# Optimization experiments

Measured on AMD Instinct MI355X. Metric: run time of the kernel, lower is better.

The kernel has to match this reference:

```python
import jax, jax.numpy as jnp
import numpy as np

NH = 8          # num_heads
NEG = -1e30     # mask_logits fill value


def setup_inputs() -> dict:
    key = jax.random.key(0)
    k1, k2, k3, k4 = jax.random.split(key, 4)
    B, D, T = 4, 1024, 2048
    x = jax.random.normal(k1, (B, D, T), dtype=jnp.float32)
    mask = jax.random.randint(k2, (B, T), 0, 2).astype(jnp.float32)
    # xavier-uniform-ish linear weights, torch layout [out, in]
    lim = float(np.sqrt(6.0 / (D + D)))
    Wq = jax.random.uniform(k3, (D, D), dtype=jnp.float32, minval=-lim, maxval=lim)
    Wo = jax.random.uniform(k4, (D, D), dtype=jnp.float32, minval=-lim, maxval=lim)
    return {"x": x, "mask": mask, "Wq": Wq, "Wo": Wo}


def reference(x, mask, Wq, Wo):
    # x: [B, D, T] channels-first; mask: [B, T] in {0,1} float
    B, D, T = x.shape
    dk = D // NH
    scale = 1.0 / jnp.sqrt(jnp.asarray(dk, x.dtype))
    xt = jnp.transpose(x, (0, 2, 1))                 # [B, T, D]
    # NOTE: original source uses Wqs for Q, K and V (source bug, reproduced)
    q = xt @ Wq.T                                    # [B, T, D]
    qh = q.reshape(B, T, NH, dk).transpose(0, 2, 1, 3)  # [B, H, T, dk]
    scores = scale * jnp.einsum('bhqd,bhkd->bhqk', qh, qh)  # [B, H, T, T]
    cmask = mask[:, None, None, :]                   # column mask [B,1,1,T]
    rmask = mask[:, None, :, None]                   # row mask    [B,1,T,1]
    logits = (scores * cmask + (1.0 - cmask) * NEG) * rmask
    attn = jax.nn.softmax(logits, axis=-1)
    ctx = jnp.einsum('bhqk,bhkd->bhqd', attn, qh)    # [B, H, T, dk]
    ctx = ctx.transpose(0, 2, 1, 3).reshape(B, T, D)
    out = ctx @ Wo.T                                 # [B, T, D]
    return jnp.transpose(out, (0, 2, 1))             # [B, D, T]
```

## Files before the change

kernel.cpp:

```cpp
#include <hip/hip_runtime.h>

#define TT 2048
#define DD 1024
#define NHH 8
#define DKK 128
#define SCALE2 0.1275174724f

typedef __attribute__((ext_vector_type(8)))  short short8;
typedef __attribute__((ext_vector_type(4)))  short short4v;
typedef __attribute__((ext_vector_type(4)))  float float4v;
typedef __attribute__((ext_vector_type(16))) float float16v;
typedef __attribute__((ext_vector_type(4)))  int   int4v;

__device__ __forceinline__ short f2bf(float f) {
  union { float f; unsigned u; } v; v.f = f;
  unsigned r = v.u + 0x7FFFu + ((v.u >> 16) & 1u);
  return (short)(r >> 16);
}
__device__ __forceinline__ unsigned cvtpk(float lo, float hi) {
  unsigned r;
  asm("v_cvt_pk_bf16_f32 %0, %1, %2" : "=v"(r) : "v"(lo), "v"(hi));
  return r;
}
__device__ __forceinline__ float xhalf_add(float x) {
  float y;
  asm("v_mov_b32 %0, %1" : "=v"(y) : "v"(x));
  asm("v_permlane32_swap_b32 %0, %1" : "+v"(x), "+v"(y));
  return x + y;
}
__device__ __forceinline__ int s4(int row) {
  return (row & 7) ^ (((row >> 3) & 3) << 2);
}
__device__ __forceinline__ void gl2lds(const void* g, void* l) {
  __builtin_amdgcn_global_load_lds(
      (const __attribute__((address_space(1))) void*)g,
      (__attribute__((address_space(3))) void*)l, 16, 0, 0);
}

__global__ __launch_bounds__(256) void k_xt(const float* __restrict__ x,
                                            short* __restrict__ xt) {
  __shared__ float tile[32][33];
  int b = blockIdx.z, d0 = blockIdx.y << 5, t0 = blockIdx.x << 5;
  int tx = threadIdx.x & 31, ty = threadIdx.x >> 5;
  const float* xp = x + ((size_t)b * DD + d0) * TT + t0;
#pragma unroll
  for (int yy = 0; yy < 32; yy += 8)
    tile[ty + yy][tx] = xp[(size_t)(ty + yy) * TT + tx];
  __syncthreads();
  short* op = xt + ((size_t)b * TT + t0) * DD + d0;
#pragma unroll
  for (int yy = 0; yy < 32; yy += 8)
    op[(size_t)(ty + yy) * DD + tx] = f2bf(tile[tx][ty + yy]);
}

__global__ void k_cast(const float* __restrict__ w, short* __restrict__ o, int n4) {
  int i = blockIdx.x * 256 + threadIdx.x;
  if (i < n4) {
    float4v v = ((const float4v*)w)[i];
    short4v s;
#pragma unroll
    for (int j = 0; j < 4; ++j) s[j] = f2bf(v[j]);
    ((short4v*)o)[i] = s;
  }
}

__global__ __launch_bounds__(256) void k_qt(const short* __restrict__ qb,
                                            short* __restrict__ qhT) {
  __shared__ short tile[64][65];
  int b = blockIdx.z, n0 = blockIdx.y << 6, t0 = blockIdx.x << 6;
  int tx = threadIdx.x & 63, ty = threadIdx.x >> 6;
  const short* ip = qb + ((size_t)(b * TT + t0)) * DD + n0;
#pragma unroll
  for (int yy = 0; yy < 64; yy += 4)
    tile[ty + yy][tx] = ip[(size_t)(ty + yy) * DD + tx];
  __syncthreads();
  short* op = qhT + ((size_t)(b * DD + n0)) * TT + t0;
#pragma unroll
  for (int yy = 0; yy < 64; yy += 4)
    op[(size_t)(ty + yy) * TT + tx] = tile[tx][ty + yy];
}

template <int EPI>
__global__ __launch_bounds__(256) void k_gemm(const short* __restrict__ A,
                                              const short* __restrict__ Bt,
                                              void* __restrict__ Cout) {
  __shared__ __align__(16) short As[128 * 64];
  __shared__ __align__(16) short Bs[128 * 64];
  const int K = 1024;
  int tm = blockIdx.x * 128, tn = blockIdx.y * 128;
  int tid = threadIdx.x, lane = tid & 63, w = tid >> 6;
  int wm = (w >> 1) * 64, wn = (w & 1) * 64;
  int ql = lane & 15, g = lane >> 4;

  int srow[4], scol[4];
#pragma unroll
  for (int c = 0; c < 4; ++c) {
    int cg = w * 4 + c;
    int r = cg * 8 + (lane >> 3);
    srow[c] = r;
    scol[c] = ((lane & 7) ^ (r & 7)) * 8;
  }

  float4v acc[4][4];
#pragma unroll
  for (int mt = 0; mt < 4; ++mt)
#pragma unroll
    for (int nt = 0; nt < 4; ++nt) acc[mt][nt] = (float4v){0.f, 0.f, 0.f, 0.f};

  for (int k0 = 0; k0 < K; k0 += 64) {
    __syncthreads();
#pragma unroll
    for (int c = 0; c < 4; ++c) {
      int cg = w * 4 + c;
      gl2lds(A + (size_t)(tm + srow[c]) * K + k0 + scol[c], As + cg * 512);
      gl2lds(Bt + (size_t)(tn + srow[c]) * K + k0 + scol[c], Bs + cg * 512);
    }
    __syncthreads();
#pragma unroll
    for (int k4 = 0; k4 < 2; ++k4) {
      short8 af[4], bfr[4];
#pragma unroll
      for (int mt = 0; mt < 4; ++mt) {
        int row = wm + mt * 16 + ql;
        af[mt] = *(const short8*)(As + row * 64 + (((k4 * 4 + g) ^ (ql & 7)) * 8));
      }
#pragma unroll
      for (int nt = 0; nt < 4; ++nt) {
        int row = wn + nt * 16 + ql;
        bfr[nt] = *(const short8*)(Bs + row * 64 + (((k4 * 4 + g) ^ (ql & 7)) * 8));
      }
#pragma unroll
      for (int mt = 0; mt < 4; ++mt)
#pragma unroll
        for (int nt = 0; nt < 4; ++nt)
          acc[mt][nt] = __builtin_amdgcn_mfma_f32_16x16x32_bf16(af[mt], bfr[nt],
                                                                acc[mt][nt], 0, 0, 0);
    }
  }

#pragma unroll
  for (int mt = 0; mt < 4; ++mt)
#pragma unroll
    for (int nt = 0; nt < 4; ++nt)
#pragma unroll
      for (int r = 0; r < 4; ++r) {
        int m = tm + wm + mt * 16 + g * 4 + r;
        int n = tn + wn + nt * 16 + ql;
        float v = acc[mt][nt][r];
        if (EPI == 0) {
          ((short*)Cout)[(size_t)m * 1024 + n] = f2bf(v);
        } else {
          int b = n >> 11, t = n & 2047;
          ((float*)Cout)[((size_t)b * 1024 + m) * 2048 + t] = v;
        }
      }
}

__global__ __launch_bounds__(256, 2) void k_attn(const short* __restrict__ q,
                                                 const short* __restrict__ qhT,
                                                 const float* __restrict__ mask,
                                                 short* __restrict__ ctx) {
  __shared__ __align__(16) short Ks[2][64 * 128];
  __shared__ __align__(16) short Vt[2][128 * 64];
  __shared__ __align__(16) short Kx[2][64 * 16];

  int qt = blockIdx.x, bh = blockIdx.y;
  int b = bh >> 3, h = bh & 7;
  int tid = threadIdx.x, lane = tid & 63, w = tid >> 6;
  int ql32 = lane & 31, hi = lane >> 5;
  int csw = s4(ql32);
  int vsw = ql32 & 7;
  short negbig = f2bf(-1e30f);

  int qrow = qt * 128 + w * 32 + ql32;
  const short* qp = q + ((size_t)(b * TT + qrow)) * DD + h * DKK;
  short8 qf[8];
#pragma unroll
  for (int kc8 = 0; kc8 < 8; ++kc8)
    qf[kc8] = *(const short8*)(qp + kc8 * 16 + hi * 8);
  float rm = mask[(size_t)b * TT + qrow];

  float qs = SCALE2 * rm;
#pragma unroll
  for (int kc8 = 0; kc8 < 8; ++kc8) {
    union { short8 s; unsigned u[4]; } a;
    a.s = qf[kc8];
#pragma unroll
    for (int j = 0; j < 4; ++j) {
      union { unsigned u; float f; } lo, hh;
      lo.u = a.u[j] << 16;
      hh.u = a.u[j] & 0xFFFF0000u;
      a.u[j] = cvtpk(lo.f * qs, hh.f * qs);
    }
    qf[kc8] = a.s;
  }
  short8 bext = (short8)0;
  if (hi == 0) bext[0] = (rm != 0.f) ? (short)0x3F80 : (short)0;

  int oc = tid & 15, r2 = tid >> 4;
  const short* kbase_g = q + ((size_t)b * TT) * DD + h * DKK + oc * 8;
  const short* vbase_g = qhT + ((size_t)(b * DD + h * DKK)) * TT;
  int vd[4], vko[4], vwoff[4];
#pragma unroll
  for (int p = 0; p < 4; ++p) {
    int idx = p * 256 + tid;
    vd[p] = idx >> 3;
    vko[p] = idx & 7;
    vwoff[p] = vd[p] * 64 + ((vko[p] ^ (vd[p] & 7)) * 8);
  }
  int kwoff[2][2];
#pragma unroll
  for (int ps = 0; ps < 2; ++ps) {
    int ra = 2 * r2 + 32 * ps, rb = ra + 1;
    kwoff[ps][0] = ra * 128 + ((oc ^ s4(ra)) * 8);
    kwoff[ps][1] = rb * 128 + ((oc ^ s4(rb)) * 8);
  }

  short8 va[2], vb[2], vv[4];
#pragma unroll
  for (int ps = 0; ps < 2; ++ps) {
    const short* kp = kbase_g + (size_t)(2 * r2 + 32 * ps) * DD;
    va[ps] = *(const short8*)(kp);
    vb[ps] = *(const short8*)(kp + DD);
  }
#pragma unroll
  for (int p = 0; p < 4; ++p)
    vv[p] = *(const short8*)(vbase_g + (size_t)vd[p] * TT + vko[p] * 8);
  float mreg = mask[(size_t)b * TT + lane];

#pragma unroll
  for (int ps = 0; ps < 2; ++ps) {
    *(short8*)(Ks[0] + kwoff[ps][0]) = va[ps];
    *(short8*)(Ks[0] + kwoff[ps][1]) = vb[ps];
  }
#pragma unroll
  for (int p = 0; p < 4; ++p)
    *(short8*)(Vt[0] + vwoff[p]) = vv[p];
  if (tid < 128) {
    short8 z = (short8)0;
    if (tid < 64) z[0] = (mreg != 0.f) ? (short)0 : negbig;
    *(short8*)(&Kx[0][0] + tid * 16) = z;
    *(short8*)(&Kx[0][0] + tid * 16 + 8) = (short8)0;
  }

  float l_run = 0.f;
  float16v o[4];
#pragma unroll
  for (int nt = 0; nt < 4; ++nt)
#pragma unroll
    for (int r = 0; r < 16; ++r) o[nt][r] = 0.f;

  for (int kt = 0; kt < 32; ++kt) {
    int cur = kt & 1;
    const short* ksb = Ks[cur];
    const short* vtb = Vt[cur];
    const short* kxb = Kx[cur];
    short* ksn = Ks[cur ^ 1];
    short* vtn = Vt[cur ^ 1];
    short* kxn = Kx[cur ^ 1];

    __syncthreads();

    if (kt < 31) {
      int kb0n = (kt + 1) * 64;
      const short* kpn = kbase_g + (size_t)kb0n * DD;
#pragma unroll
      for (int ps = 0; ps < 2; ++ps) {
        const short* kp = kpn + (size_t)(2 * r2 + 32 * ps) * DD;
        va[ps] = *(const short8*)(kp);
        vb[ps] = *(const short8*)(kp + DD);
      }
#pragma unroll
      for (int p = 0; p < 4; ++p)
        vv[p] = *(const short8*)(vbase_g + (size_t)vd[p] * TT + kb0n + vko[p] * 8);
      mreg = mask[(size_t)b * TT + kb0n + lane];
    }

    float16v st0, st1;
#pragma unroll
    for (int r = 0; r < 16; ++r) { st0[r] = 0.f; st1[r] = 0.f; }
    __builtin_amdgcn_s_setprio(1);
    {
      short8 ax0 = *(const short8*)(kxb + ql32 * 16 + hi * 8);
      short8 ax1 = *(const short8*)(kxb + (32 + ql32) * 16 + hi * 8);
      st0 = __builtin_amdgcn_mfma_f32_32x32x16_bf16(ax0, bext, st0, 0, 0, 0);
      st1 = __builtin_amdgcn_mfma_f32_32x32x16_bf16(ax1, bext, st1, 0, 0, 0);
    }
#pragma unroll
    for (int kc8 = 0; kc8 < 8; ++kc8) {
      int csk = ((kc8 * 2 + hi) ^ csw) * 8;
      short8 kf0 = *(const short8*)(ksb + ql32 * 128 + csk);
      short8 kf1 = *(const short8*)(ksb + (32 + ql32) * 128 + csk);
      st0 = __builtin_amdgcn_mfma_f32_32x32x16_bf16(kf0, qf[kc8], st0, 0, 0, 0);
      st1 = __builtin_amdgcn_mfma_f32_32x32x16_bf16(kf1, qf[kc8], st1, 0, 0, 0);
    }
    __builtin_amdgcn_s_setprio(0);

    float tsum = 0.f;
#pragma unroll
    for (int r = 0; r < 16; ++r) {
      float p0 = __builtin_amdgcn_exp2f(st0[r]);
      float p1 = __builtin_amdgcn_exp2f(st1[r]);
      st0[r] = p0; st1[r] = p1;
      tsum += p0 + p1;
    }
    l_run += xhalf_add(tsum);

    short8 pa[4];
#pragma unroll
    for (int kc = 0; kc < 4; ++kc) {
      int a0 = 2 * (kc & 1);
      unsigned x0, x1, y0, y1;
      if (kc < 2) {
        x0 = cvtpk(st0[4 * a0 + 0], st0[4 * a0 + 1]);
        x1 = cvtpk(st0[4 * a0 + 2], st0[4 * a0 + 3]);
        y0 = cvtpk(st0[4 * a0 + 4], st0[4 * a0 + 5]);
        y1 = cvtpk(st0[4 * a0 + 6], st0[4 * a0 + 7]);
      } else {
        x0 = cvtpk(st1[4 * a0 + 0], st1[4 * a0 + 1]);
        x1 = cvtpk(st1[4 * a0 + 2], st1[4 * a0 + 3]);
        y0 = cvtpk(st1[4 * a0 + 4], st1[4 * a0 + 5]);
        y1 = cvtpk(st1[4 * a0 + 6], st1[4 * a0 + 7]);
      }
      asm("v_permlane32_swap_b32 %0, %1" : "+v"(x0), "+v"(y0));
      asm("v_permlane32_swap_b32 %0, %1" : "+v"(x1), "+v"(y1));
      union { unsigned u[4]; short8 s8; } pu;
      pu.u[0] = x0; pu.u[1] = x1; pu.u[2] = y0; pu.u[3] = y1;
      pa[kc] = pu.s8;
    }

    __builtin_amdgcn_s_setprio(1);
#pragma unroll
    for (int nt = 0; nt < 4; ++nt) {
      int row = nt * 32 + ql32;
#pragma unroll
      for (int kc = 0; kc < 4; ++kc) {
        short8 vf = *(const short8*)(vtb + row * 64 + (((kc * 2 + hi) ^ vsw) * 8));
        o[nt] = __builtin_amdgcn_mfma_f32_32x32x16_bf16(vf, pa[kc], o[nt], 0, 0, 0);
      }
    }
    __builtin_amdgcn_s_setprio(0);

    if (kt < 31) {
#pragma unroll
      for (int ps = 0; ps < 2; ++ps) {
        *(short8*)(ksn + kwoff[ps][0]) = va[ps];
        *(short8*)(ksn + kwoff[ps][1]) = vb[ps];
      }
#pragma unroll
      for (int p = 0; p < 4; ++p)
        *(short8*)(vtn + vwoff[p]) = vv[p];
      if (tid < 64) {
        unsigned word = (mreg != 0.f) ? 0u : (unsigned)(unsigned short)negbig;
        *(unsigned*)(kxn + tid * 16) = word;
      }
    }
  }

  float il = 1.0f / l_run;
  short* cp = ctx + ((size_t)(b * TT + qrow)) * DD + h * DKK;
#pragma unroll
  for (int nt = 0; nt < 4; ++nt)
#pragma unroll
    for (int a = 0; a < 4; ++a) {
      short4v sv;
#pragma unroll
      for (int j = 0; j < 4; ++j) sv[j] = f2bf(o[nt][4 * a + j] * il);
      *(short4v*)(cp + nt * 32 + 8 * a + 4 * hi) = sv;
    }
}

extern "C" void kernel_launch(void* const* d_in, const int* in_sizes, int n_in,
                              void* d_out, int out_size, void* d_ws, size_t ws_size,
                              hipStream_t stream) {
  const float* x    = (const float*)d_in[0];
  const float* mask = (const float*)d_in[1];
  const float* Wq   = (const float*)d_in[2];
  const float* Wo   = (const float*)d_in[3];
  char* ws = (char*)d_ws;
  short* xt  = (short*)(ws);
  short* wqb = (short*)(ws + (size_t)16 * 1024 * 1024);
  short* wob = (short*)(ws + (size_t)18 * 1024 * 1024);
  short* qb  = (short*)(ws + (size_t)20 * 1024 * 1024);
  short* ctx = (short*)(ws + (size_t)36 * 1024 * 1024);
  short* qhT = xt;

  k_xt<<<dim3(64, 32, 4), 256, 0, stream>>>(x, xt);
  k_cast<<<1024, 256, 0, stream>>>(Wq, wqb, 262144);
  k_cast<<<1024, 256, 0, stream>>>(Wo, wob, 262144);
  k_gemm<0><<<dim3(64, 8), 256, 0, stream>>>(xt, wqb, qb);
  k_qt<<<dim3(32, 16, 4), 256, 0, stream>>>(qb, qhT);
  k_attn<<<dim3(16, 32), 256, 0, stream>>>(qb, qhT, mask, ctx);
  k_gemm<1><<<dim3(8, 64), 256, 0, stream>>>(wob, ctx, d_out);
}
```

Baseline: 148.2 us.

## Fuse prep kernels and emit transposed Q from the projection GEMM epilogue

Merges the x-transpose and the two weight casts into one launch by splitting on block index. The Q-projection GEMM now stages its bf16 tile in LDS and writes both row-major Q with vectorized stores and the transposed qhT, which removes the separate transpose kernel and its extra read of Q. This saves two launches and one pass over Q, at the cost of roughly 34KB more LDS in the GEMM, which may reduce occupancy, plus strided LDS reads in the transposed store.

```diff
diff --git a/kernel.cpp b/kernel.cpp
--- a/kernel.cpp
+++ b/kernel.cpp
@@ -37,55 +37,47 @@
       (__attribute__((address_space(3))) void*)l, 16, 0, 0);
 }
 
-__global__ __launch_bounds__(256) void k_xt(const float* __restrict__ x,
-                                            short* __restrict__ xt) {
-  __shared__ float tile[32][33];
-  int b = blockIdx.z, d0 = blockIdx.y << 5, t0 = blockIdx.x << 5;
-  int tx = threadIdx.x & 31, ty = threadIdx.x >> 5;
-  const float* xp = x + ((size_t)b * DD + d0) * TT + t0;
-#pragma unroll
-  for (int yy = 0; yy < 32; yy += 8)
-    tile[ty + yy][tx] = xp[(size_t)(ty + yy) * TT + tx];
-  __syncthreads();
-  short* op = xt + ((size_t)b * TT + t0) * DD + d0;
-#pragma unroll
-  for (int yy = 0; yy < 32; yy += 8)
-    op[(size_t)(ty + yy) * DD + tx] = f2bf(tile[tx][ty + yy]);
-}
-
-__global__ void k_cast(const float* __restrict__ w, short* __restrict__ o, int n4) {
-  int i = blockIdx.x * 256 + threadIdx.x;
-  if (i < n4) {
+__global__ __launch_bounds__(256) void k_prep(const float* __restrict__ x,
+                                              short* __restrict__ xt,
+                                              const float* __restrict__ Wq,
+                                              short* __restrict__ wqb,
+                                              const float* __restrict__ Wo,
+                                              short* __restrict__ wob) {
+  int id = blockIdx.x;
+  if (id < 8192) {
+    __shared__ float tile[32][33];
+    int ttile = id & 63, dtile = (id >> 6) & 31, b = id >> 11;
+    int d0 = dtile << 5, t0 = ttile << 5;
+    int tx = threadIdx.x & 31, ty = threadIdx.x >> 5;
+    const float* xp = x + ((size_t)b * DD + d0) * TT + t0;
+#pragma unroll
+    for (int yy = 0; yy < 32; yy += 8)
+      tile[ty + yy][tx] = xp[(size_t)(ty + yy) * TT + tx];
+    __syncthreads();
+    short* op = xt + ((size_t)b * TT + t0) * DD + d0;
+#pragma unroll
+    for (int yy = 0; yy < 32; yy += 8)
+      op[(size_t)(ty + yy) * DD + tx] = f2bf(tile[tx][ty + yy]);
+  } else {
+    const float* w = (id < 9216) ? Wq : Wo;
+    short* o = (id < 9216) ? wqb : wob;
+    int i = (id - 8192 - ((id < 9216) ? 0 : 1024)) * 256 + threadIdx.x;
     float4v v = ((const float4v*)w)[i];
     short4v s;
 #pragma unroll
     for (int j = 0; j < 4; ++j) s[j] = f2bf(v[j]);
     ((short4v*)o)[i] = s;
   }
-}
-
-__global__ __launch_bounds__(256) void k_qt(const short* __restrict__ qb,
-                                            short* __restrict__ qhT) {
-  __shared__ short tile[64][65];
-  int b = blockIdx.z, n0 = blockIdx.y << 6, t0 = blockIdx.x << 6;
-  int tx = threadIdx.x & 63, ty = threadIdx.x >> 6;
-  const short* ip = qb + ((size_t)(b * TT + t0)) * DD + n0;
-#pragma unroll
-  for (int yy = 0; yy < 64; yy += 4)
-    tile[ty + yy][tx] = ip[(size_t)(ty + yy) * DD + tx];
-  __syncthreads();
-  short* op = qhT + ((size_t)(b * DD + n0)) * TT + t0;
-#pragma unroll
-  for (int yy = 0; yy < 64; yy += 4)
-    op[(size_t)(ty + yy) * TT + tx] = tile[tx][ty + yy];
 }
 
 template <int EPI>
 __global__ __launch_bounds__(256) void k_gemm(const short* __restrict__ A,
                                               const short* __restrict__ Bt,
-                                              void* __restrict__ Cout) {
+                                              void* __restrict__ Cout,
+                                              short* __restrict__ qhT) {
   __shared__ __align__(16) short As[128 * 64];
   __shared__ __align__(16) short Bs[128 * 64];
+  __shared__ __align__(16) short Ct[(EPI == 0) ? 128 * 136 : 1];
   const int K = 1024;
   int tm = blockIdx.x * 128, tn = blockIdx.y * 128;
   int tid = threadIdx.x, lane = tid & 63, w = tid >> 6;
@@ -138,22 +130,51 @@
     }
   }
 
-#pragma unroll
-  for (int mt = 0; mt < 4; ++mt)
-#pragma unroll
-    for (int nt = 0; nt < 4; ++nt)
-#pragma unroll
-      for (int r = 0; r < 4; ++r) {
-        int m = tm + wm + mt * 16 + g * 4 + r;
-        int n = tn + wn + nt * 16 + ql;
-        float v = acc[mt][nt][r];
-        if (EPI == 0) {
-          ((short*)Cout)[(size_t)m * 1024 + n] = f2bf(v);
-        } else {
+  if (EPI == 1) {
+#pragma unroll
+    for (int mt = 0; mt < 4; ++mt)
+#pragma unroll
+      for (int nt = 0; nt < 4; ++nt)
+#pragma unroll
+        for (int r = 0; r < 4; ++r) {
+          int m = tm + wm + mt * 16 + g * 4 + r;
+          int n = tn + wn + nt * 16 + ql;
           int b = n >> 11, t = n & 2047;
-          ((float*)Cout)[((size_t)b * 1024 + m) * 2048 + t] = v;
+          ((float*)Cout)[((size_t)b * 1024 + m) * 2048 + t] = acc[mt][nt][r];
         }
-      }
+  } else {
+    __syncthreads();
+#pragma unroll
+    for (int mt = 0; mt < 4; ++mt)
+#pragma unroll
+      for (int nt = 0; nt < 4; ++nt)
+#pragma unroll
+        for (int r = 0; r < 4; ++r)
+          Ct[(wm + mt * 16 + g * 4 + r) * 136 + wn + nt * 16 + ql] =
+              f2bf(acc[mt][nt][r]);
+    __syncthreads();
+    int bb = tm >> 11, t0 = tm & 2047;
+    short* qb = (short*)Cout;
+    {
+      int m = tid >> 1, c0 = (tid & 1) * 64;
+      short* dst = qb + (size_t)(tm + m) * 1024 + tn + c0;
+      const short* src = Ct + m * 136 + c0;
+#pragma unroll
+      for (int i = 0; i < 8; ++i)
+        *(short8*)(dst + i * 8) = *(const short8*)(src + i * 8);
+    }
+    {
+      int n = tid >> 1, m0 = (tid & 1) * 64;
+      short* dst = qhT + ((size_t)(bb * DD + tn + n)) * TT + t0 + m0;
+#pragma unroll
+      for (int i = 0; i < 8; ++i) {
+        short8 v;
+#pragma unroll
+        for (int j = 0; j < 8; ++j) v[j] = Ct[(m0 + i * 8 + j) * 136 + n];
+        *(short8*)(dst + i * 8) = v;
+      }
+    }
+  }
 }
 
 __global__ __launch_bounds__(256, 2) void k_attn(const short* __restrict__ q,
@@ -383,13 +404,10 @@
   short* wob = (short*)(ws + (size_t)18 * 1024 * 1024);
   short* qb  = (short*)(ws + (size_t)20 * 1024 * 1024);
   short* ctx = (short*)(ws + (size_t)36 * 1024 * 1024);
-  short* qhT = xt;
-
-  k_xt<<<dim3(64, 32, 4), 256, 0, stream>>>(x, xt);
-  k_cast<<<1024, 256, 0, stream>>>(Wq, wqb, 262144);
-  k_cast<<<1024, 256, 0, stream>>>(Wo, wob, 262144);
-  k_gemm<0><<<dim3(64, 8), 256, 0, stream>>>(xt, wqb, qb);
-  k_qt<<<dim3(32, 16, 4), 256, 0, stream>>>(qb, qhT);
+  short* qhT = (short*)(ws + (size_t)52 * 1024 * 1024);
+
+  k_prep<<<10240, 256, 0, stream>>>(x, xt, Wq, wqb, Wo, wob);
+  k_gemm<0><<<dim3(64, 8), 256, 0, stream>>>(xt, wqb, qb, qhT);
   k_attn<<<dim3(16, 32), 256, 0, stream>>>(qb, qhT, mask, ctx);
-  k_gemm<1><<<dim3(8, 64), 256, 0, stream>>>(wob, ctx, d_out);
-}
+  k_gemm<1><<<dim3(8, 64), 256, 0, stream>>>(wob, ctx, d_out, nullptr);
+}
```

After: 149.7 us. No clear change (+1.0%).
